# Kernel tuning notes

Hardware: AMD Instinct MI355X
Metric: run time of the kernel (lower is better)

## Reference

```python
import jax, jax.numpy as jnp
import numpy as np

# Model dims
B, S, D = 4, 2048, 2048   # batch, seq, emb_dim
E, K, M = 8, 2, 1024      # num_experts, num_experts_per_tok, intermediate_dim


def setup_inputs() -> dict:
    key = jax.random.key(0)
    k0, k1, k2, k3, k4 = jax.random.split(key, 5)
    d_scale = D ** -0.5
    m_scale = M ** -0.5
    return {
        "x": jax.random.normal(k0, (B, S, D), jnp.float32),
        "w_gate": jax.random.normal(k1, (D, E), jnp.float32) * d_scale,
        "wi_0": jax.random.normal(k2, (E, D, M), jnp.float32) * d_scale,  # gate proj per expert
        "wi_1": jax.random.normal(k3, (E, D, M), jnp.float32) * d_scale,  # up proj per expert
        "wo": jax.random.normal(k4, (E, M, D), jnp.float32) * m_scale,    # down proj per expert
    }


def reference(x, w_gate, wi_0, wi_1, wo):
    b, s, d = x.shape
    e = w_gate.shape[1]
    xf = x.reshape(-1, d)                       # [T, D], T = B*S
    # --- gate logits + top-k routing ---
    logits = jnp.dot(xf, w_gate)                # [T, E]
    top_logits, top_idx = jax.lax.top_k(logits, K)    # [T, K]
    weights = jax.nn.softmax(top_logits, axis=-1)     # [T, K] router weights
    # --- sort token copies by assigned expert (dispatch) ---
    flat_idx = top_idx.reshape(-1)              # [T*K] expert id per token copy
    sort_order = jnp.argsort(flat_idx)          # [T*K] dispatch permutation
    token_ids = sort_order // K                 # source token for each sorted slot
    sorted_x = jnp.take(xf, token_ids, axis=0)  # [T*K, D] gathered activations
    group_sizes = jnp.bincount(flat_idx, length=E).astype(jnp.int32)  # tokens per expert
    # --- grouped expert GEMMs (silu-gated MLP) ---
    h0 = jax.lax.ragged_dot(sorted_x, wi_0, group_sizes)  # [T*K, M]
    h1 = jax.lax.ragged_dot(sorted_x, wi_1, group_sizes)  # [T*K, M]
    inter = jax.nn.silu(h0) * h1
    out_sorted = jax.lax.ragged_dot(inter, wo, group_sizes)  # [T*K, D]
    # --- unsort + weighted combine ---
    unsort = jnp.argsort(sort_order)
    out = jnp.take(out_sorted, unsort, axis=0).reshape(-1, K, d)  # [T, K, D]
    out = jnp.einsum("tkd,tk->td", out, weights)
    return out.reshape(b, s, d)
```

## Files before the change

kernel.cpp:

```cpp
#include <hip/hip_runtime.h>
#include <hip/hip_bf16.h>
#include <math.h>

#define T_TOK 8192
#define DIM   2048
#define NE    8
#define MDIM  1024
#define TK    16384
#define CAP   (TK + 256)
#define MAXT  72

typedef __attribute__((ext_vector_type(8))) short bf16x8;
typedef __attribute__((ext_vector_type(4))) float f32x4;

typedef __attribute__((address_space(3))) unsigned char* lds_ptr_t;
typedef const __attribute__((address_space(1))) unsigned char* glb_ptr_t;

__device__ __forceinline__ unsigned short f2bf(float f) {
  union { float f; unsigned u; } v; v.f = f;
  unsigned r = v.u + 0x7fffu + ((v.u >> 16) & 1u);
  return (unsigned short)(r >> 16);
}

__device__ __forceinline__ void gload_lds16(const void* g, void* l) {
  __builtin_amdgcn_global_load_lds((glb_ptr_t)g, (lds_ptr_t)l, 16, 0, 0);
}

#define VM_FENCE(n) asm volatile("s_waitcnt vmcnt(" #n ")" ::: "memory")
#define BARRIER() __builtin_amdgcn_s_barrier()

__device__ __forceinline__ void stage_unit(const unsigned short* __restrict__ src,
                                           int ld, unsigned char* lds, int tid) {
#pragma unroll
  for (int j = 0; j < 2; j++) {
    int idx = j * 512 + tid;
    int row = idx >> 3;
    int gslot = (idx & 7) ^ (row & 7);
    gload_lds16(src + (size_t)row * ld + gslot * 8, lds + ((idx & ~63) << 4));
  }
}

__device__ __forceinline__ bf16x8 ldsfrag(const unsigned char* base, int row, int kb) {
  return *(const bf16x8*)(base + row * 128 + (kb ^ ((row & 7) << 4)));
}

__global__ __launch_bounds__(256) void router_kernel(
    const float* __restrict__ x, const float* __restrict__ wg,
    int* __restrict__ tok_eid, float* __restrict__ tok_w) {
  __shared__ float wgT[NE][1024];
  int tid = threadIdx.x;
  int wave = tid >> 6, lane = tid & 63;
  int t0 = blockIdx.x * 16 + wave * 4;

  double acc[4][NE];
#pragma unroll
  for (int tt = 0; tt < 4; tt++)
#pragma unroll
    for (int e = 0; e < NE; e++) acc[tt][e] = 0.0;

  for (int p = 0; p < 2; p++) {
    __syncthreads();
#pragma unroll
    for (int j = tid; j < 2048; j += 256) {
      float4 v = ((const float4*)wg)[p * 2048 + j];
      int d = j >> 1, h = (j & 1) * 4;
      wgT[h + 0][d] = v.x;
      wgT[h + 1][d] = v.y;
      wgT[h + 2][d] = v.z;
      wgT[h + 3][d] = v.w;
    }
    __syncthreads();
#pragma unroll
    for (int it = 0; it < 4; it++) {
      int dd = it * 256 + lane * 4;
      int gd = p * 1024 + dd;
      float4 wf[NE];
#pragma unroll
      for (int e = 0; e < NE; e++) wf[e] = *(const float4*)&wgT[e][dd];
#pragma unroll
      for (int tt = 0; tt < 4; tt++) {
        float4 xv = *(const float4*)(x + (size_t)(t0 + tt) * DIM + gd);
#pragma unroll
        for (int e = 0; e < NE; e++) {
          acc[tt][e] += (double)xv.x * (double)wf[e].x;
          acc[tt][e] += (double)xv.y * (double)wf[e].y;
          acc[tt][e] += (double)xv.z * (double)wf[e].z;
          acc[tt][e] += (double)xv.w * (double)wf[e].w;
        }
      }
    }
  }
#pragma unroll
  for (int tt = 0; tt < 4; tt++)
#pragma unroll
    for (int e = 0; e < NE; e++) {
      double v = acc[tt][e];
#pragma unroll
      for (int off = 32; off > 0; off >>= 1) v += __shfl_down(v, off, 64);
      acc[tt][e] = v;
    }
  if (lane == 0) {
#pragma unroll
    for (int tt = 0; tt < 4; tt++) {
      int t = t0 + tt;
      int b0 = 0; double l0 = acc[tt][0];
#pragma unroll
      for (int e = 1; e < NE; e++) { if (acc[tt][e] > l0) { l0 = acc[tt][e]; b0 = e; } }
      int b1 = -1; double l1 = -1.0e300;
#pragma unroll
      for (int e = 0; e < NE; e++) { if (e != b0 && acc[tt][e] > l1) { l1 = acc[tt][e]; b1 = e; } }
      double w0 = 1.0 / (1.0 + exp(l1 - l0));
      tok_eid[2 * t]     = b0;
      tok_eid[2 * t + 1] = b1;
      tok_w[2 * t]     = (float)w0;
      tok_w[2 * t + 1] = (float)(1.0 - w0);
    }
  }
}

__global__ __launch_bounds__(256) void plan_kernel(
    const int* __restrict__ tok_eid, int* __restrict__ offsets,
    int* __restrict__ tstart, int* __restrict__ tok_slot) {
  __shared__ int cnt[256][NE];
  __shared__ int pre[256][NE];
  __shared__ int tot[NE];
  __shared__ int off_sh[NE + 1];
  int th = threadIdx.x;
  int c[NE];
#pragma unroll
  for (int k = 0; k < NE; k++) c[k] = 0;
  for (int i = 0; i < TK / 256; i++) {
    int e = tok_eid[i * 256 + th];
#pragma unroll
    for (int k = 0; k < NE; k++) c[k] += (e == k) ? 1 : 0;
  }
#pragma unroll
  for (int k = 0; k < NE; k++) cnt[th][k] = c[k];
  __syncthreads();
  if (th < NE) {
    int run = 0;
#pragma unroll 4
    for (int i = 0; i < 256; i++) { pre[i][th] = run; run += cnt[i][th]; }
    tot[th] = run;
  }
  __syncthreads();
  if (th == 0) {
    int s = 0, ts = 0;
    for (int e = 0; e < NE; e++) {
      off_sh[e] = s; offsets[e] = s; s += tot[e];
      tstart[e] = ts; ts += (tot[e] + 255) / 256;
    }
    offsets[NE] = s; off_sh[NE] = s; tstart[NE] = ts;
  }
  __syncthreads();
  int b[NE];
#pragma unroll
  for (int k = 0; k < NE; k++) b[k] = off_sh[k] + pre[th][k];
  for (int i = 0; i < TK / 256; i++) {
    int idx = i * 256 + th;
    int e = tok_eid[idx];
    int slot = 0;
#pragma unroll
    for (int k = 0; k < NE; k++) {
      slot = (e == k) ? b[k] : slot;
      b[k] += (e == k) ? 1 : 0;
    }
    tok_slot[idx] = slot;
  }
}

__global__ __launch_bounds__(256) void dispatch_kernel(
    const float* __restrict__ x, const int* __restrict__ tok_slot,
    unsigned short* __restrict__ sorted_x) {
  int t = blockIdx.x;
  size_t s0 = (size_t)tok_slot[2 * t] * DIM;
  size_t s1 = (size_t)tok_slot[2 * t + 1] * DIM;
  const float4* xr = (const float4*)(x + (size_t)t * DIM);
#pragma unroll
  for (int i = threadIdx.x; i < DIM / 4; i += 256) {
    float4 v = xr[i];
    ushort4 b;
    b.x = f2bf(v.x); b.y = f2bf(v.y); b.z = f2bf(v.z); b.w = f2bf(v.w);
    *(ushort4*)(sorted_x + s0 + (size_t)i * 4) = b;
    *(ushort4*)(sorted_x + s1 + (size_t)i * 4) = b;
  }
}

__global__ __launch_bounds__(256) void transpose_cast_kernel(
    const float* __restrict__ in, unsigned short* __restrict__ out, int R, int C) {
  __shared__ unsigned short tile[32][33];
  int e = blockIdx.z;
  const float* inp = in + (size_t)e * R * C;
  unsigned short* outp = out + (size_t)e * R * C;
  int c0 = blockIdx.x * 32, r0 = blockIdx.y * 32;
  int tx = threadIdx.x & 31, ty = threadIdx.x >> 5;
#pragma unroll
  for (int i = 0; i < 32; i += 8)
    tile[ty + i][tx] = f2bf(inp[(size_t)(r0 + ty + i) * C + (c0 + tx)]);
  __syncthreads();
#pragma unroll
  for (int i = 0; i < 32; i += 8)
    outp[(size_t)(c0 + ty + i) * R + (r0 + tx)] = tile[tx][ty + i];
}

__global__ __launch_bounds__(512, 2) void gemm12_kernel(
    const unsigned short* __restrict__ A, const unsigned short* __restrict__ W0t,
    const unsigned short* __restrict__ W1t, const int* __restrict__ offsets,
    const int* __restrict__ tstart, unsigned short* __restrict__ inter) {
  extern __shared__ unsigned char smem[];
  int bx = blockIdx.x;
  if (bx >= tstart[NE]) return;
  int e = 0;
#pragma unroll
  for (int k = 1; k < NE; k++) if (tstart[k] <= bx) e = k;
  int row0 = offsets[e], row_end = offsets[e + 1];
  int tile_r0 = row0 + (bx - tstart[e]) * 256;
  if (tile_r0 >= row_end) return;
  int colb = blockIdx.y * 128;

  int tid = threadIdx.x;
  int wave = tid >> 6, lane = tid & 63;
  int wm = wave >> 2, wn = wave & 3;
  int l15 = lane & 15, grp16 = (lane >> 4) * 16;

  const unsigned short* Ab = A + (size_t)tile_r0 * DIM;
  const unsigned short* B0b = W0t + ((size_t)e * MDIM + colb) * DIM;
  const unsigned short* B1b = W1t + ((size_t)e * MDIM + colb) * DIM;

  f32x4 acc0[8][2], acc1[8][2];
#pragma unroll
  for (int i = 0; i < 8; i++)
#pragma unroll
    for (int j = 0; j < 2; j++) {
      acc0[i][j] = (f32x4){0.f, 0.f, 0.f, 0.f};
      acc1[i][j] = (f32x4){0.f, 0.f, 0.f, 0.f};
    }
  bf16x8 af[4][2], b0f[2][2], b1f[2][2];

  stage_unit(Ab, DIM, smem + 0, tid);
  stage_unit(B0b, DIM, smem + 32768, tid);
  stage_unit(B1b, DIM, smem + 49152, tid);
  stage_unit(Ab + (size_t)128 * DIM, DIM, smem + 16384, tid);
  VM_FENCE(4);
  BARRIER();

  for (int t = 0; t < 32; t++) {
    unsigned char* S = smem + (t & 1) * 65536;
    unsigned char* P = smem + ((t & 1) ^ 1) * 65536;
    int kn = (t < 31 ? t + 1 : t) * 64;
#pragma unroll
    for (int mi = 0; mi < 4; mi++) {
      int r = wm * 64 + mi * 16 + l15;
#pragma unroll
      for (int ks = 0; ks < 2; ks++) af[mi][ks] = ldsfrag(S, r, ks * 64 + grp16);
    }
#pragma unroll
    for (int ni = 0; ni < 2; ni++) {
      int r = wn * 32 + ni * 16 + l15;
#pragma unroll
      for (int ks = 0; ks < 2; ks++) b0f[ni][ks] = ldsfrag(S + 32768, r, ks * 64 + grp16);
    }
    stage_unit(Ab + kn, DIM, P, tid);
    BARRIER();
    __builtin_amdgcn_s_setprio(1);
#pragma unroll
    for (int ks = 0; ks < 2; ks++)
#pragma unroll
      for (int mi = 0; mi < 4; mi++)
#pragma unroll
        for (int ni = 0; ni < 2; ni++)
          acc0[mi][ni] = __builtin_amdgcn_mfma_f32_16x16x32_bf16(af[mi][ks], b0f[ni][ks], acc0[mi][ni], 0, 0, 0);
    __builtin_amdgcn_s_setprio(0);
    VM_FENCE(4);
    BARRIER();
#pragma unroll
    for (int ni = 0; ni < 2; ni++) {
      int r = wn * 32 + ni * 16 + l15;
#pragma unroll
      for (int ks = 0; ks < 2; ks++) b1f[ni][ks] = ldsfrag(S + 49152, r, ks * 64 + grp16);
    }
    stage_unit(B0b + kn, DIM, P + 32768, tid);
    BARRIER();
    __builtin_amdgcn_s_setprio(1);
#pragma unroll
    for (int ks = 0; ks < 2; ks++)
#pragma unroll
      for (int mi = 0; mi < 4; mi++)
#pragma unroll
        for (int ni = 0; ni < 2; ni++)
          acc1[mi][ni] = __builtin_amdgcn_mfma_f32_16x16x32_bf16(af[mi][ks], b1f[ni][ks], acc1[mi][ni], 0, 0, 0);
    __builtin_amdgcn_s_setprio(0);
    VM_FENCE(4);
    BARRIER();
#pragma unroll
    for (int mi = 0; mi < 4; mi++) {
      int r = 128 + wm * 64 + mi * 16 + l15;
#pragma unroll
      for (int ks = 0; ks < 2; ks++) af[mi][ks] = ldsfrag(S, r, ks * 64 + grp16);
    }
    stage_unit(B1b + kn, DIM, P + 49152, tid);
    BARRIER();
    __builtin_amdgcn_s_setprio(1);
#pragma unroll
    for (int ks = 0; ks < 2; ks++)
#pragma unroll
      for (int mi = 0; mi < 4; mi++)
#pragma unroll
        for (int ni = 0; ni < 2; ni++)
          acc0[4 + mi][ni] = __builtin_amdgcn_mfma_f32_16x16x32_bf16(af[mi][ks], b0f[ni][ks], acc0[4 + mi][ni], 0, 0, 0);
    __builtin_amdgcn_s_setprio(0);
    BARRIER();
    stage_unit(Ab + (size_t)128 * DIM + kn, DIM, P + 16384, tid);
    BARRIER();
    __builtin_amdgcn_s_setprio(1);
#pragma unroll
    for (int ks = 0; ks < 2; ks++)
#pragma unroll
      for (int mi = 0; mi < 4; mi++)
#pragma unroll
        for (int ni = 0; ni < 2; ni++)
          acc1[4 + mi][ni] = __builtin_amdgcn_mfma_f32_16x16x32_bf16(af[mi][ks], b1f[ni][ks], acc1[4 + mi][ni], 0, 0, 0);
    __builtin_amdgcn_s_setprio(0);
    VM_FENCE(4);
    BARRIER();
  }
  VM_FENCE(0);

#pragma unroll
  for (int half = 0; half < 2; half++)
#pragma unroll
    for (int mi = 0; mi < 4; mi++)
#pragma unroll
      for (int reg = 0; reg < 4; reg++) {
        int grow = tile_r0 + half * 128 + wm * 64 + mi * 16 + (lane >> 4) * 4 + reg;
        if (grow < row_end) {
#pragma unroll
          for (int ni = 0; ni < 2; ni++) {
            float h0 = acc0[half * 4 + mi][ni][reg];
            float h1 = acc1[half * 4 + mi][ni][reg];
            float g = h0 / (1.0f + __expf(-h0));
            inter[(size_t)grow * MDIM + colb + wn * 32 + ni * 16 + l15] = f2bf(g * h1);
          }
        }
      }
}

__global__ __launch_bounds__(512, 2) void gemm3_kernel(
    const unsigned short* __restrict__ A, const unsigned short* __restrict__ Wot,
    const int* __restrict__ offsets, const int* __restrict__ tstart,
    float* __restrict__ out_sorted) {
  extern __shared__ unsigned char smem[];
  int bx = blockIdx.x;
  if (bx >= tstart[NE]) return;
  int e = 0;
#pragma unroll
  for (int k = 1; k < NE; k++) if (tstart[k] <= bx) e = k;
  int row0 = offsets[e], row_end = offsets[e + 1];
  int tile_r0 = row0 + (bx - tstart[e]) * 256;
  if (tile_r0 >= row_end) return;
  int col0 = blockIdx.y * 256;

  int tid = threadIdx.x;
  int wave = tid >> 6, lane = tid & 63;
  int wm = wave >> 2, wn = wave & 3;
  int l15 = lane & 15, grp16 = (lane >> 4) * 16;

  const unsigned short* Ab = A + (size_t)tile_r0 * MDIM;
  const unsigned short* Bb = Wot + ((size_t)e * DIM + col0) * MDIM;

  f32x4 acc[8][4];
#pragma unroll
  for (int i = 0; i < 8; i++)
#pragma unroll
    for (int j = 0; j < 4; j++) acc[i][j] = (f32x4){0.f, 0.f, 0.f, 0.f};
  bf16x8 af[4][2], bfr[4][2];

  stage_unit(Ab, MDIM, smem + 0, tid);
  stage_unit(Bb, MDIM, smem + 32768, tid);
  stage_unit(Bb + (size_t)128 * MDIM, MDIM, smem + 49152, tid);
  stage_unit(Ab + (size_t)128 * MDIM, MDIM, smem + 16384, tid);
  VM_FENCE(4);
  BARRIER();

  for (int t = 0; t < 16; t++) {
    unsigned char* S = smem + (t & 1) * 65536;
    unsigned char* P = smem + ((t & 1) ^ 1) * 65536;
    int kn = (t < 15 ? t + 1 : t) * 64;
#pragma unroll
    for (int mi = 0; mi < 4; mi++) {
      int r = wm * 64 + mi * 16 + l15;
#pragma unroll
      for (int ks = 0; ks < 2; ks++) af[mi][ks] = ldsfrag(S, r, ks * 64 + grp16);
    }
#pragma unroll
    for (int ni = 0; ni < 2; ni++) {
      int r = wn * 32 + ni * 16 + l15;
#pragma unroll
      for (int ks = 0; ks < 2; ks++) bfr[ni][ks] = ldsfrag(S + 32768, r, ks * 64 + grp16);
    }
    stage_unit(Ab + kn, MDIM, P, tid);
    BARRIER();
    __builtin_amdgcn_s_setprio(1);
#pragma unroll
    for (int ks = 0; ks < 2; ks++)
#pragma unroll
      for (int mi = 0; mi < 4; mi++)
#pragma unroll
        for (int ni = 0; ni < 2; ni++)
          acc[mi][ni] = __builtin_amdgcn_mfma_f32_16x16x32_bf16(af[mi][ks], bfr[ni][ks], acc[mi][ni], 0, 0, 0);
    __builtin_amdgcn_s_setprio(0);
    VM_FENCE(4);
    BARRIER();
#pragma unroll
    for (int ni = 0; ni < 2; ni++) {
      int r = 128 + wn * 32 + ni * 16 + l15;
#pragma unroll
      for (int ks = 0; ks < 2; ks++) bfr[2 + ni][ks] = ldsfrag(S + 32768, r, ks * 64 + grp16);
    }
    stage_unit(Bb + kn, MDIM, P + 32768, tid);
    BARRIER();
    __builtin_amdgcn_s_setprio(1);
#pragma unroll
    for (int ks = 0; ks < 2; ks++)
#pragma unroll
      for (int mi = 0; mi < 4; mi++)
#pragma unroll
        for (int ni = 0; ni < 2; ni++)
          acc[mi][2 + ni] = __builtin_amdgcn_mfma_f32_16x16x32_bf16(af[mi][ks], bfr[2 + ni][ks], acc[mi][2 + ni], 0, 0, 0);
    __builtin_amdgcn_s_setprio(0);
    VM_FENCE(4);
    BARRIER();
#pragma unroll
    for (int mi = 0; mi < 4; mi++) {
      int r = 128 + wm * 64 + mi * 16 + l15;
#pragma unroll
      for (int ks = 0; ks < 2; ks++) af[mi][ks] = ldsfrag(S, r, ks * 64 + grp16);
    }
    stage_unit(Bb + (size_t)128 * MDIM + kn, MDIM, P + 49152, tid);
    BARRIER();
    __builtin_amdgcn_s_setprio(1);
#pragma unroll
    for (int ks = 0; ks < 2; ks++)
#pragma unroll
      for (int mi = 0; mi < 4; mi++)
#pragma unroll
        for (int ni = 0; ni < 2; ni++)
          acc[4 + mi][ni] = __builtin_amdgcn_mfma_f32_16x16x32_bf16(af[mi][ks], bfr[ni][ks], acc[4 + mi][ni], 0, 0, 0);
    __builtin_amdgcn_s_setprio(0);
    BARRIER();
    stage_unit(Ab + (size_t)128 * MDIM + kn, MDIM, P + 16384, tid);
    BARRIER();
    __builtin_amdgcn_s_setprio(1);
#pragma unroll
    for (int ks = 0; ks < 2; ks++)
#pragma unroll
      for (int mi = 0; mi < 4; mi++)
#pragma unroll
        for (int ni = 0; ni < 2; ni++)
          acc[4 + mi][2 + ni] = __builtin_amdgcn_mfma_f32_16x16x32_bf16(af[mi][ks], bfr[2 + ni][ks], acc[4 + mi][2 + ni], 0, 0, 0);
    __builtin_amdgcn_s_setprio(0);
    VM_FENCE(4);
    BARRIER();
  }
  VM_FENCE(0);

#pragma unroll
  for (int mh = 0; mh < 2; mh++)
#pragma unroll
    for (int mi = 0; mi < 4; mi++)
#pragma unroll
      for (int reg = 0; reg < 4; reg++) {
        int grow = tile_r0 + mh * 128 + wm * 64 + mi * 16 + (lane >> 4) * 4 + reg;
        if (grow < row_end) {
#pragma unroll
          for (int nh = 0; nh < 2; nh++) {
            float* orow = out_sorted + (size_t)grow * DIM + col0 + nh * 128 + wn * 32 + l15;
#pragma unroll
            for (int ni = 0; ni < 2; ni++)
              orow[ni * 16] = acc[mh * 4 + mi][nh * 2 + ni][reg];
          }
        }
      }
}

__global__ __launch_bounds__(256) void combine_kernel(
    const float* __restrict__ os, const int* __restrict__ tok_slot,
    const float* __restrict__ tok_w, float* __restrict__ out) {
  int t = blockIdx.x * 4 + (threadIdx.x >> 6);
  int lane = threadIdx.x & 63;
  int s0 = tok_slot[2 * t], s1 = tok_slot[2 * t + 1];
  float w0 = tok_w[2 * t], w1 = tok_w[2 * t + 1];
  const float4* a = (const float4*)(os + (size_t)s0 * DIM);
  const float4* b = (const float4*)(os + (size_t)s1 * DIM);
  float4* o = (float4*)(out + (size_t)t * DIM);
#pragma unroll
  for (int i = lane; i < DIM / 4; i += 64) {
    float4 va = a[i], vb = b[i];
    float4 r;
    r.x = w0 * va.x + w1 * vb.x;
    r.y = w0 * va.y + w1 * vb.y;
    r.z = w0 * va.z + w1 * vb.z;
    r.w = w0 * va.w + w1 * vb.w;
    o[i] = r;
  }
}

extern "C" void kernel_launch(void* const* d_in, const int* in_sizes, int n_in,
                              void* d_out, int out_size, void* d_ws, size_t ws_size,
                              hipStream_t stream) {
  const float* x   = (const float*)d_in[0];
  const float* wg  = (const float*)d_in[1];
  const float* wi0 = (const float*)d_in[2];
  const float* wi1 = (const float*)d_in[3];
  const float* wo  = (const float*)d_in[4];
  float* out = (float*)d_out;

  (void)hipFuncSetAttribute(reinterpret_cast<const void*>(gemm12_kernel),
                            hipFuncAttributeMaxDynamicSharedMemorySize, 131072);
  (void)hipFuncSetAttribute(reinterpret_cast<const void*>(gemm3_kernel),
                            hipFuncAttributeMaxDynamicSharedMemorySize, 131072);

  char* ws = (char*)d_ws;
  size_t off = 0;
  auto alloc = [&](size_t bytes) -> void* {
    void* p = ws + off;
    off = (off + bytes + 255) & ~(size_t)255;
    return p;
  };
  int*   offsets  = (int*)alloc((NE + 1) * 4);
  int*   tstart   = (int*)alloc((NE + 1) * 4);
  int*   tok_eid  = (int*)alloc((size_t)2 * T_TOK * 4);
  float* tok_w    = (float*)alloc((size_t)2 * T_TOK * 4);
  int*   tok_slot = (int*)alloc((size_t)2 * T_TOK * 4);
  unsigned short* inter    = (unsigned short*)alloc((size_t)CAP * MDIM * 2);
  unsigned short* sorted_x = (unsigned short*)alloc((size_t)CAP * DIM * 2);
  unsigned short* W0t      = (unsigned short*)alloc((size_t)NE * MDIM * DIM * 2);
  unsigned short* W1t      = (unsigned short*)alloc((size_t)NE * MDIM * DIM * 2);
  unsigned short* Wot      = (unsigned short*)alloc((size_t)NE * DIM * MDIM * 2);
  float* out_sorted = (float*)sorted_x;

  router_kernel<<<T_TOK / 16, 256, 0, stream>>>(x, wg, tok_eid, tok_w);
  plan_kernel<<<1, 256, 0, stream>>>(tok_eid, offsets, tstart, tok_slot);
  dispatch_kernel<<<T_TOK, 256, 0, stream>>>(x, tok_slot, sorted_x);
  transpose_cast_kernel<<<dim3(MDIM / 32, DIM / 32, NE), 256, 0, stream>>>(wi0, W0t, DIM, MDIM);
  transpose_cast_kernel<<<dim3(MDIM / 32, DIM / 32, NE), 256, 0, stream>>>(wi1, W1t, DIM, MDIM);
  transpose_cast_kernel<<<dim3(DIM / 32, MDIM / 32, NE), 256, 0, stream>>>(wo, Wot, MDIM, DIM);

  gemm12_kernel<<<dim3(MAXT, MDIM / 128, 1), 512, 131072, stream>>>(
      sorted_x, W0t, W1t, offsets, tstart, inter);
  gemm3_kernel<<<dim3(MAXT, DIM / 256, 1), 512, 131072, stream>>>(
      inter, Wot, offsets, tstart, out_sorted);
  combine_kernel<<<T_TOK / 4, 256, 0, stream>>>(out_sorted, tok_slot, tok_w, out);
}
```

Before: 614.7 us.

## Split tail row tiles into 64-row sub-tiles to balance the expert GEMM wave

Both expert GEMM kernels now launch on a flat 1D grid. The first 512 blocks cover row tiles 0-63 with the original 256-row pipelined path. Row tiles 64 and up, the per-expert padding overflow, are handled by blocks that each compute a 64-row quarter tile with a simpler single-stage double-buffered loop. The aim is to shrink the second wave of full-size tiles that ran after the first 512 blocks filled the device. In exchange the tail blocks reuse weights less and use a less overlapped load/compute schedule.

Result: faster. 590.3 us (-4.0%).

```diff
diff --git a/kernel.cpp b/kernel.cpp
--- a/kernel.cpp
+++ b/kernel.cpp
@@ -8,7 +8,6 @@
 #define MDIM  1024
 #define TK    16384
 #define CAP   (TK + 256)
-#define MAXT  72
 
 typedef __attribute__((ext_vector_type(8))) short bf16x8;
 typedef __attribute__((ext_vector_type(4))) float f32x4;
@@ -38,6 +37,13 @@
     int gslot = (idx & 7) ^ (row & 7);
     gload_lds16(src + (size_t)row * ld + gslot * 8, lds + ((idx & ~63) << 4));
   }
+}
+
+__device__ __forceinline__ void stage_unit64(const unsigned short* __restrict__ src,
+                                             int ld, unsigned char* lds, int tid) {
+  int row = tid >> 3;
+  int gslot = (tid & 7) ^ (row & 7);
+  gload_lds16(src + (size_t)row * ld + gslot * 8, lds + ((tid & ~63) << 4));
 }
 
 __device__ __forceinline__ bf16x8 ldsfrag(const unsigned char* base, int row, int kb) {
@@ -209,140 +215,226 @@
     const int* __restrict__ tstart, unsigned short* __restrict__ inter) {
   extern __shared__ unsigned char smem[];
   int bx = blockIdx.x;
-  if (bx >= tstart[NE]) return;
-  int e = 0;
-#pragma unroll
-  for (int k = 1; k < NE; k++) if (tstart[k] <= bx) e = k;
-  int row0 = offsets[e], row_end = offsets[e + 1];
-  int tile_r0 = row0 + (bx - tstart[e]) * 256;
-  if (tile_r0 >= row_end) return;
-  int colb = blockIdx.y * 128;
-
   int tid = threadIdx.x;
   int wave = tid >> 6, lane = tid & 63;
   int wm = wave >> 2, wn = wave & 3;
   int l15 = lane & 15, grp16 = (lane >> 4) * 16;
 
-  const unsigned short* Ab = A + (size_t)tile_r0 * DIM;
-  const unsigned short* B0b = W0t + ((size_t)e * MDIM + colb) * DIM;
-  const unsigned short* B1b = W1t + ((size_t)e * MDIM + colb) * DIM;
-
-  f32x4 acc0[8][2], acc1[8][2];
-#pragma unroll
-  for (int i = 0; i < 8; i++)
-#pragma unroll
-    for (int j = 0; j < 2; j++) {
-      acc0[i][j] = (f32x4){0.f, 0.f, 0.f, 0.f};
-      acc1[i][j] = (f32x4){0.f, 0.f, 0.f, 0.f};
-    }
-  bf16x8 af[4][2], b0f[2][2], b1f[2][2];
-
-  stage_unit(Ab, DIM, smem + 0, tid);
-  stage_unit(B0b, DIM, smem + 32768, tid);
-  stage_unit(B1b, DIM, smem + 49152, tid);
-  stage_unit(Ab + (size_t)128 * DIM, DIM, smem + 16384, tid);
-  VM_FENCE(4);
-  BARRIER();
-
-  for (int t = 0; t < 32; t++) {
-    unsigned char* S = smem + (t & 1) * 65536;
-    unsigned char* P = smem + ((t & 1) ^ 1) * 65536;
-    int kn = (t < 31 ? t + 1 : t) * 64;
-#pragma unroll
-    for (int mi = 0; mi < 4; mi++) {
-      int r = wm * 64 + mi * 16 + l15;
-#pragma unroll
-      for (int ks = 0; ks < 2; ks++) af[mi][ks] = ldsfrag(S, r, ks * 64 + grp16);
-    }
-#pragma unroll
-    for (int ni = 0; ni < 2; ni++) {
-      int r = wn * 32 + ni * 16 + l15;
-#pragma unroll
-      for (int ks = 0; ks < 2; ks++) b0f[ni][ks] = ldsfrag(S + 32768, r, ks * 64 + grp16);
-    }
-    stage_unit(Ab + kn, DIM, P, tid);
-    BARRIER();
-    __builtin_amdgcn_s_setprio(1);
-#pragma unroll
-    for (int ks = 0; ks < 2; ks++)
-#pragma unroll
-      for (int mi = 0; mi < 4; mi++)
-#pragma unroll
-        for (int ni = 0; ni < 2; ni++)
-          acc0[mi][ni] = __builtin_amdgcn_mfma_f32_16x16x32_bf16(af[mi][ks], b0f[ni][ks], acc0[mi][ni], 0, 0, 0);
-    __builtin_amdgcn_s_setprio(0);
+  if (bx < 512) {
+    int rt = bx >> 3;
+    int colb = (bx & 7) * 128;
+    int e = 0;
+#pragma unroll
+    for (int k = 1; k < NE; k++) if (tstart[k] <= rt) e = k;
+    int row_end = offsets[e + 1];
+    int tile_r0 = offsets[e] + (rt - tstart[e]) * 256;
+
+    const unsigned short* Ab = A + (size_t)tile_r0 * DIM;
+    const unsigned short* B0b = W0t + ((size_t)e * MDIM + colb) * DIM;
+    const unsigned short* B1b = W1t + ((size_t)e * MDIM + colb) * DIM;
+
+    f32x4 acc0[8][2], acc1[8][2];
+#pragma unroll
+    for (int i = 0; i < 8; i++)
+#pragma unroll
+      for (int j = 0; j < 2; j++) {
+        acc0[i][j] = (f32x4){0.f, 0.f, 0.f, 0.f};
+        acc1[i][j] = (f32x4){0.f, 0.f, 0.f, 0.f};
+      }
+    bf16x8 af[4][2], b0f[2][2], b1f[2][2];
+
+    stage_unit(Ab, DIM, smem + 0, tid);
+    stage_unit(B0b, DIM, smem + 32768, tid);
+    stage_unit(B1b, DIM, smem + 49152, tid);
+    stage_unit(Ab + (size_t)128 * DIM, DIM, smem + 16384, tid);
     VM_FENCE(4);
     BARRIER();
-#pragma unroll
-    for (int ni = 0; ni < 2; ni++) {
-      int r = wn * 32 + ni * 16 + l15;
-#pragma unroll
-      for (int ks = 0; ks < 2; ks++) b1f[ni][ks] = ldsfrag(S + 49152, r, ks * 64 + grp16);
-    }
-    stage_unit(B0b + kn, DIM, P + 32768, tid);
-    BARRIER();
-    __builtin_amdgcn_s_setprio(1);
-#pragma unroll
-    for (int ks = 0; ks < 2; ks++)
+
+    for (int t = 0; t < 32; t++) {
+      unsigned char* S = smem + (t & 1) * 65536;
+      unsigned char* P = smem + ((t & 1) ^ 1) * 65536;
+      int kn = (t < 31 ? t + 1 : t) * 64;
+#pragma unroll
+      for (int mi = 0; mi < 4; mi++) {
+        int r = wm * 64 + mi * 16 + l15;
+#pragma unroll
+        for (int ks = 0; ks < 2; ks++) af[mi][ks] = ldsfrag(S, r, ks * 64 + grp16);
+      }
+#pragma unroll
+      for (int ni = 0; ni < 2; ni++) {
+        int r = wn * 32 + ni * 16 + l15;
+#pragma unroll
+        for (int ks = 0; ks < 2; ks++) b0f[ni][ks] = ldsfrag(S + 32768, r, ks * 64 + grp16);
+      }
+      stage_unit(Ab + kn, DIM, P, tid);
+      BARRIER();
+      __builtin_amdgcn_s_setprio(1);
+#pragma unroll
+      for (int ks = 0; ks < 2; ks++)
+#pragma unroll
+        for (int mi = 0; mi < 4; mi++)
+#pragma unroll
+          for (int ni = 0; ni < 2; ni++)
+            acc0[mi][ni] = __builtin_amdgcn_mfma_f32_16x16x32_bf16(af[mi][ks], b0f[ni][ks], acc0[mi][ni], 0, 0, 0);
+      __builtin_amdgcn_s_setprio(0);
+      VM_FENCE(4);
+      BARRIER();
+#pragma unroll
+      for (int ni = 0; ni < 2; ni++) {
+        int r = wn * 32 + ni * 16 + l15;
+#pragma unroll
+        for (int ks = 0; ks < 2; ks++) b1f[ni][ks] = ldsfrag(S + 49152, r, ks * 64 + grp16);
+      }
+      stage_unit(B0b + kn, DIM, P + 32768, tid);
+      BARRIER();
+      __builtin_amdgcn_s_setprio(1);
+#pragma unroll
+      for (int ks = 0; ks < 2; ks++)
+#pragma unroll
+        for (int mi = 0; mi < 4; mi++)
+#pragma unroll
+          for (int ni = 0; ni < 2; ni++)
+            acc1[mi][ni] = __builtin_amdgcn_mfma_f32_16x16x32_bf16(af[mi][ks], b1f[ni][ks], acc1[mi][ni], 0, 0, 0);
+      __builtin_amdgcn_s_setprio(0);
+      VM_FENCE(4);
+      BARRIER();
+#pragma unroll
+      for (int mi = 0; mi < 4; mi++) {
+        int r = 128 + wm * 64 + mi * 16 + l15;
+#pragma unroll
+        for (int ks = 0; ks < 2; ks++) af[mi][ks] = ldsfrag(S, r, ks * 64 + grp16);
+      }
+      stage_unit(B1b + kn, DIM, P + 49152, tid);
+      BARRIER();
+      __builtin_amdgcn_s_setprio(1);
+#pragma unroll
+      for (int ks = 0; ks < 2; ks++)
+#pragma unroll
+        for (int mi = 0; mi < 4; mi++)
+#pragma unroll
+          for (int ni = 0; ni < 2; ni++)
+            acc0[4 + mi][ni] = __builtin_amdgcn_mfma_f32_16x16x32_bf16(af[mi][ks], b0f[ni][ks], acc0[4 + mi][ni], 0, 0, 0);
+      __builtin_amdgcn_s_setprio(0);
+      BARRIER();
+      stage_unit(Ab + (size_t)128 * DIM + kn, DIM, P + 16384, tid);
+      BARRIER();
+      __builtin_amdgcn_s_setprio(1);
+#pragma unroll
+      for (int ks = 0; ks < 2; ks++)
+#pragma unroll
+        for (int mi = 0; mi < 4; mi++)
+#pragma unroll
+          for (int ni = 0; ni < 2; ni++)
+            acc1[4 + mi][ni] = __builtin_amdgcn_mfma_f32_16x16x32_bf16(af[mi][ks], b1f[ni][ks], acc1[4 + mi][ni], 0, 0, 0);
+      __builtin_amdgcn_s_setprio(0);
+      VM_FENCE(4);
+      BARRIER();
+    }
+    VM_FENCE(0);
+
+#pragma unroll
+    for (int half = 0; half < 2; half++)
 #pragma unroll
       for (int mi = 0; mi < 4; mi++)
 #pragma unroll
-        for (int ni = 0; ni < 2; ni++)
-          acc1[mi][ni] = __builtin_amdgcn_mfma_f32_16x16x32_bf16(af[mi][ks], b1f[ni][ks], acc1[mi][ni], 0, 0, 0);
-    __builtin_amdgcn_s_setprio(0);
-    VM_FENCE(4);
-    BARRIER();
-#pragma unroll
-    for (int mi = 0; mi < 4; mi++) {
-      int r = 128 + wm * 64 + mi * 16 + l15;
-#pragma unroll
-      for (int ks = 0; ks < 2; ks++) af[mi][ks] = ldsfrag(S, r, ks * 64 + grp16);
-    }
-    stage_unit(B1b + kn, DIM, P + 49152, tid);
-    BARRIER();
-    __builtin_amdgcn_s_setprio(1);
-#pragma unroll
-    for (int ks = 0; ks < 2; ks++)
-#pragma unroll
-      for (int mi = 0; mi < 4; mi++)
-#pragma unroll
-        for (int ni = 0; ni < 2; ni++)
-          acc0[4 + mi][ni] = __builtin_amdgcn_mfma_f32_16x16x32_bf16(af[mi][ks], b0f[ni][ks], acc0[4 + mi][ni], 0, 0, 0);
-    __builtin_amdgcn_s_setprio(0);
-    BARRIER();
-    stage_unit(Ab + (size_t)128 * DIM + kn, DIM, P + 16384, tid);
-    BARRIER();
-    __builtin_amdgcn_s_setprio(1);
-#pragma unroll
-    for (int ks = 0; ks < 2; ks++)
-#pragma unroll
-      for (int mi = 0; mi < 4; mi++)
-#pragma unroll
-        for (int ni = 0; ni < 2; ni++)
-          acc1[4 + mi][ni] = __builtin_amdgcn_mfma_f32_16x16x32_bf16(af[mi][ks], b1f[ni][ks], acc1[4 + mi][ni], 0, 0, 0);
-    __builtin_amdgcn_s_setprio(0);
-    VM_FENCE(4);
-    BARRIER();
-  }
-  VM_FENCE(0);
-
-#pragma unroll
-  for (int half = 0; half < 2; half++)
-#pragma unroll
-    for (int mi = 0; mi < 4; mi++)
-#pragma unroll
-      for (int reg = 0; reg < 4; reg++) {
-        int grow = tile_r0 + half * 128 + wm * 64 + mi * 16 + (lane >> 4) * 4 + reg;
-        if (grow < row_end) {
-#pragma unroll
-          for (int ni = 0; ni < 2; ni++) {
-            float h0 = acc0[half * 4 + mi][ni][reg];
-            float h1 = acc1[half * 4 + mi][ni][reg];
-            float g = h0 / (1.0f + __expf(-h0));
-            inter[(size_t)grow * MDIM + colb + wn * 32 + ni * 16 + l15] = f2bf(g * h1);
+        for (int reg = 0; reg < 4; reg++) {
+          int grow = tile_r0 + half * 128 + wm * 64 + mi * 16 + (lane >> 4) * 4 + reg;
+          if (grow < row_end) {
+#pragma unroll
+            for (int ni = 0; ni < 2; ni++) {
+              float h0 = acc0[half * 4 + mi][ni][reg];
+              float h1 = acc1[half * 4 + mi][ni][reg];
+              float g = h0 / (1.0f + __expf(-h0));
+              inter[(size_t)grow * MDIM + colb + wn * 32 + ni * 16 + l15] = f2bf(g * h1);
+            }
           }
         }
-      }
+  } else {
+    int g = bx - 512;
+    int rt = 64 + (g >> 5);
+    if (rt >= tstart[NE]) return;
+    int q = (g >> 3) & 3;
+    int colb = (g & 7) * 128;
+    int e = 0;
+#pragma unroll
+    for (int k = 1; k < NE; k++) if (tstart[k] <= rt) e = k;
+    int row_end = offsets[e + 1];
+    int tr0 = offsets[e] + (rt - tstart[e]) * 256 + q * 64;
+    if (tr0 >= row_end) return;
+
+    const unsigned short* Ab = A + (size_t)tr0 * DIM;
+    const unsigned short* B0b = W0t + ((size_t)e * MDIM + colb) * DIM;
+    const unsigned short* B1b = W1t + ((size_t)e * MDIM + colb) * DIM;
+
+    f32x4 acc0[2][2], acc1[2][2];
+#pragma unroll
+    for (int i = 0; i < 2; i++)
+#pragma unroll
+      for (int j = 0; j < 2; j++) {
+        acc0[i][j] = (f32x4){0.f, 0.f, 0.f, 0.f};
+        acc1[i][j] = (f32x4){0.f, 0.f, 0.f, 0.f};
+      }
+    bf16x8 af[2][2], b0f[2][2], b1f[2][2];
+
+    stage_unit64(Ab, DIM, smem + 0, tid);
+    stage_unit(B0b, DIM, smem + 16384, tid);
+    stage_unit(B1b, DIM, smem + 49152, tid);
+    VM_FENCE(0);
+    BARRIER();
+
+    for (int t = 0; t < 32; t++) {
+      unsigned char* S = smem + (t & 1) * 65536;
+      unsigned char* P = smem + ((t & 1) ^ 1) * 65536;
+      int kn = (t < 31 ? t + 1 : t) * 64;
+      stage_unit64(Ab + kn, DIM, P, tid);
+      stage_unit(B0b + kn, DIM, P + 16384, tid);
+      stage_unit(B1b + kn, DIM, P + 49152, tid);
+#pragma unroll
+      for (int mi = 0; mi < 2; mi++) {
+        int r = wm * 32 + mi * 16 + l15;
+#pragma unroll
+        for (int ks = 0; ks < 2; ks++) af[mi][ks] = ldsfrag(S, r, ks * 64 + grp16);
+      }
+#pragma unroll
+      for (int ni = 0; ni < 2; ni++) {
+        int r = wn * 32 + ni * 16 + l15;
+#pragma unroll
+        for (int ks = 0; ks < 2; ks++) {
+          b0f[ni][ks] = ldsfrag(S + 16384, r, ks * 64 + grp16);
+          b1f[ni][ks] = ldsfrag(S + 49152, r, ks * 64 + grp16);
+        }
+      }
+      __builtin_amdgcn_s_setprio(1);
+#pragma unroll
+      for (int ks = 0; ks < 2; ks++)
+#pragma unroll
+        for (int mi = 0; mi < 2; mi++)
+#pragma unroll
+          for (int ni = 0; ni < 2; ni++) {
+            acc0[mi][ni] = __builtin_amdgcn_mfma_f32_16x16x32_bf16(af[mi][ks], b0f[ni][ks], acc0[mi][ni], 0, 0, 0);
+            acc1[mi][ni] = __builtin_amdgcn_mfma_f32_16x16x32_bf16(af[mi][ks], b1f[ni][ks], acc1[mi][ni], 0, 0, 0);
+          }
+      __builtin_amdgcn_s_setprio(0);
+      VM_FENCE(0);
+      BARRIER();
+    }
+
+#pragma unroll
+    for (int mi = 0; mi < 2; mi++)
+#pragma unroll
+      for (int reg = 0; reg < 4; reg++) {
+        int grow = tr0 + wm * 32 + mi * 16 + (lane >> 4) * 4 + reg;
+        if (grow < row_end) {
+#pragma unroll
+          for (int ni = 0; ni < 2; ni++) {
+            float h0 = acc0[mi][ni][reg];
+            float h1 = acc1[mi][ni][reg];
+            float gq = h0 / (1.0f + __expf(-h0));
+            inter[(size_t)grow * MDIM + colb + wn * 32 + ni * 16 + l15] = f2bf(gq * h1);
+          }
+        }
+      }
+  }
 }
 
 __global__ __launch_bounds__(512, 2) void gemm3_kernel(
@@ -351,136 +443,211 @@
     float* __restrict__ out_sorted) {
   extern __shared__ unsigned char smem[];
   int bx = blockIdx.x;
-  if (bx >= tstart[NE]) return;
-  int e = 0;
-#pragma unroll
-  for (int k = 1; k < NE; k++) if (tstart[k] <= bx) e = k;
-  int row0 = offsets[e], row_end = offsets[e + 1];
-  int tile_r0 = row0 + (bx - tstart[e]) * 256;
-  if (tile_r0 >= row_end) return;
-  int col0 = blockIdx.y * 256;
-
   int tid = threadIdx.x;
   int wave = tid >> 6, lane = tid & 63;
   int wm = wave >> 2, wn = wave & 3;
   int l15 = lane & 15, grp16 = (lane >> 4) * 16;
 
-  const unsigned short* Ab = A + (size_t)tile_r0 * MDIM;
-  const unsigned short* Bb = Wot + ((size_t)e * DIM + col0) * MDIM;
-
-  f32x4 acc[8][4];
-#pragma unroll
-  for (int i = 0; i < 8; i++)
-#pragma unroll
-    for (int j = 0; j < 4; j++) acc[i][j] = (f32x4){0.f, 0.f, 0.f, 0.f};
-  bf16x8 af[4][2], bfr[4][2];
-
-  stage_unit(Ab, MDIM, smem + 0, tid);
-  stage_unit(Bb, MDIM, smem + 32768, tid);
-  stage_unit(Bb + (size_t)128 * MDIM, MDIM, smem + 49152, tid);
-  stage_unit(Ab + (size_t)128 * MDIM, MDIM, smem + 16384, tid);
-  VM_FENCE(4);
-  BARRIER();
-
-  for (int t = 0; t < 16; t++) {
-    unsigned char* S = smem + (t & 1) * 65536;
-    unsigned char* P = smem + ((t & 1) ^ 1) * 65536;
-    int kn = (t < 15 ? t + 1 : t) * 64;
-#pragma unroll
-    for (int mi = 0; mi < 4; mi++) {
-      int r = wm * 64 + mi * 16 + l15;
-#pragma unroll
-      for (int ks = 0; ks < 2; ks++) af[mi][ks] = ldsfrag(S, r, ks * 64 + grp16);
-    }
-#pragma unroll
-    for (int ni = 0; ni < 2; ni++) {
-      int r = wn * 32 + ni * 16 + l15;
-#pragma unroll
-      for (int ks = 0; ks < 2; ks++) bfr[ni][ks] = ldsfrag(S + 32768, r, ks * 64 + grp16);
-    }
-    stage_unit(Ab + kn, MDIM, P, tid);
-    BARRIER();
-    __builtin_amdgcn_s_setprio(1);
-#pragma unroll
-    for (int ks = 0; ks < 2; ks++)
-#pragma unroll
-      for (int mi = 0; mi < 4; mi++)
-#pragma unroll
-        for (int ni = 0; ni < 2; ni++)
-          acc[mi][ni] = __builtin_amdgcn_mfma_f32_16x16x32_bf16(af[mi][ks], bfr[ni][ks], acc[mi][ni], 0, 0, 0);
-    __builtin_amdgcn_s_setprio(0);
+  if (bx < 512) {
+    int rt = bx >> 3;
+    int col0 = (bx & 7) * 256;
+    int e = 0;
+#pragma unroll
+    for (int k = 1; k < NE; k++) if (tstart[k] <= rt) e = k;
+    int row_end = offsets[e + 1];
+    int tile_r0 = offsets[e] + (rt - tstart[e]) * 256;
+
+    const unsigned short* Ab = A + (size_t)tile_r0 * MDIM;
+    const unsigned short* Bb = Wot + ((size_t)e * DIM + col0) * MDIM;
+
+    f32x4 acc[8][4];
+#pragma unroll
+    for (int i = 0; i < 8; i++)
+#pragma unroll
+      for (int j = 0; j < 4; j++) acc[i][j] = (f32x4){0.f, 0.f, 0.f, 0.f};
+    bf16x8 af[4][2], bfr[4][2];
+
+    stage_unit(Ab, MDIM, smem + 0, tid);
+    stage_unit(Bb, MDIM, smem + 32768, tid);
+    stage_unit(Bb + (size_t)128 * MDIM, MDIM, smem + 49152, tid);
+    stage_unit(Ab + (size_t)128 * MDIM, MDIM, smem + 16384, tid);
     VM_FENCE(4);
     BARRIER();
-#pragma unroll
-    for (int ni = 0; ni < 2; ni++) {
-      int r = 128 + wn * 32 + ni * 16 + l15;
-#pragma unroll
-      for (int ks = 0; ks < 2; ks++) bfr[2 + ni][ks] = ldsfrag(S + 32768, r, ks * 64 + grp16);
-    }
-    stage_unit(Bb + kn, MDIM, P + 32768, tid);
-    BARRIER();
-    __builtin_amdgcn_s_setprio(1);
-#pragma unroll
-    for (int ks = 0; ks < 2; ks++)
+
+    for (int t = 0; t < 16; t++) {
+      unsigned char* S = smem + (t & 1) * 65536;
+      unsigned char* P = smem + ((t & 1) ^ 1) * 65536;
+      int kn = (t < 15 ? t + 1 : t) * 64;
+#pragma unroll
+      for (int mi = 0; mi < 4; mi++) {
+        int r = wm * 64 + mi * 16 + l15;
+#pragma unroll
+        for (int ks = 0; ks < 2; ks++) af[mi][ks] = ldsfrag(S, r, ks * 64 + grp16);
+      }
+#pragma unroll
+      for (int ni = 0; ni < 2; ni++) {
+        int r = wn * 32 + ni * 16 + l15;
+#pragma unroll
+        for (int ks = 0; ks < 2; ks++) bfr[ni][ks] = ldsfrag(S + 32768, r, ks * 64 + grp16);
+      }
+      stage_unit(Ab + kn, MDIM, P, tid);
+      BARRIER();
+      __builtin_amdgcn_s_setprio(1);
+#pragma unroll
+      for (int ks = 0; ks < 2; ks++)
+#pragma unroll
+        for (int mi = 0; mi < 4; mi++)
+#pragma unroll
+          for (int ni = 0; ni < 2; ni++)
+            acc[mi][ni] = __builtin_amdgcn_mfma_f32_16x16x32_bf16(af[mi][ks], bfr[ni][ks], acc[mi][ni], 0, 0, 0);
+      __builtin_amdgcn_s_setprio(0);
+      VM_FENCE(4);
+      BARRIER();
+#pragma unroll
+      for (int ni = 0; ni < 2; ni++) {
+        int r = 128 + wn * 32 + ni * 16 + l15;
+#pragma unroll
+        for (int ks = 0; ks < 2; ks++) bfr[2 + ni][ks] = ldsfrag(S + 32768, r, ks * 64 + grp16);
+      }
+      stage_unit(Bb + kn, MDIM, P + 32768, tid);
+      BARRIER();
+      __builtin_amdgcn_s_setprio(1);
+#pragma unroll
+      for (int ks = 0; ks < 2; ks++)
+#pragma unroll
+        for (int mi = 0; mi < 4; mi++)
+#pragma unroll
+          for (int ni = 0; ni < 2; ni++)
+            acc[mi][2 + ni] = __builtin_amdgcn_mfma_f32_16x16x32_bf16(af[mi][ks], bfr[2 + ni][ks], acc[mi][2 + ni], 0, 0, 0);
+      __builtin_amdgcn_s_setprio(0);
+      VM_FENCE(4);
+      BARRIER();
+#pragma unroll
+      for (int mi = 0; mi < 4; mi++) {
+        int r = 128 + wm * 64 + mi * 16 + l15;
+#pragma unroll
+        for (int ks = 0; ks < 2; ks++) af[mi][ks] = ldsfrag(S, r, ks * 64 + grp16);
+      }
+      stage_unit(Bb + (size_t)128 * MDIM + kn, MDIM, P + 49152, tid);
+      BARRIER();
+      __builtin_amdgcn_s_setprio(1);
+#pragma unroll
+      for (int ks = 0; ks < 2; ks++)
+#pragma unroll
+        for (int mi = 0; mi < 4; mi++)
+#pragma unroll
+          for (int ni = 0; ni < 2; ni++)
+            acc[4 + mi][ni] = __builtin_amdgcn_mfma_f32_16x16x32_bf16(af[mi][ks], bfr[ni][ks], acc[4 + mi][ni], 0, 0, 0);
+      __builtin_amdgcn_s_setprio(0);
+      BARRIER();
+      stage_unit(Ab + (size_t)128 * MDIM + kn, MDIM, P + 16384, tid);
+      BARRIER();
+      __builtin_amdgcn_s_setprio(1);
+#pragma unroll
+      for (int ks = 0; ks < 2; ks++)
+#pragma unroll
+        for (int mi = 0; mi < 4; mi++)
+#pragma unroll
+          for (int ni = 0; ni < 2; ni++)
+            acc[4 + mi][2 + ni] = __builtin_amdgcn_mfma_f32_16x16x32_bf16(af[mi][ks], bfr[2 + ni][ks], acc[4 + mi][2 + ni], 0, 0, 0);
+      __builtin_amdgcn_s_setprio(0);
+      VM_FENCE(4);
+      BARRIER();
+    }
+    VM_FENCE(0);
+
+#pragma unroll
+    for (int mh = 0; mh < 2; mh++)
 #pragma unroll
       for (int mi = 0; mi < 4; mi++)
 #pragma unroll
-        for (int ni = 0; ni < 2; ni++)
-          acc[mi][2 + ni] = __builtin_amdgcn_mfma_f32_16x16x32_bf16(af[mi][ks], bfr[2 + ni][ks], acc[mi][2 + ni], 0, 0, 0);
-    __builtin_amdgcn_s_setprio(0);
-    VM_FENCE(4);
-    BARRIER();
-#pragma unroll
-    for (int mi = 0; mi < 4; mi++) {
-      int r = 128 + wm * 64 + mi * 16 + l15;
-#pragma unroll
-      for (int ks = 0; ks < 2; ks++) af[mi][ks] = ldsfrag(S, r, ks * 64 + grp16);
-    }
-    stage_unit(Bb + (size_t)128 * MDIM + kn, MDIM, P + 49152, tid);
-    BARRIER();
-    __builtin_amdgcn_s_setprio(1);
-#pragma unroll
-    for (int ks = 0; ks < 2; ks++)
-#pragma unroll
-      for (int mi = 0; mi < 4; mi++)
-#pragma unroll
-        for (int ni = 0; ni < 2; ni++)
-          acc[4 + mi][ni] = __builtin_amdgcn_mfma_f32_16x16x32_bf16(af[mi][ks], bfr[ni][ks], acc[4 + mi][ni], 0, 0, 0);
-    __builtin_amdgcn_s_setprio(0);
-    BARRIER();
-    stage_unit(Ab + (size_t)128 * MDIM + kn, MDIM, P + 16384, tid);
-    BARRIER();
-    __builtin_amdgcn_s_setprio(1);
-#pragma unroll
-    for (int ks = 0; ks < 2; ks++)
-#pragma unroll
-      for (int mi = 0; mi < 4; mi++)
-#pragma unroll
-        for (int ni = 0; ni < 2; ni++)
-          acc[4 + mi][2 + ni] = __builtin_amdgcn_mfma_f32_16x16x32_bf16(af[mi][ks], bfr[2 + ni][ks], acc[4 + mi][2 + ni], 0, 0, 0);
-    __builtin_amdgcn_s_setprio(0);
-    VM_FENCE(4);
-    BARRIER();
-  }
-  VM_FENCE(0);
-
-#pragma unroll
-  for (int mh = 0; mh < 2; mh++)
-#pragma unroll
-    for (int mi = 0; mi < 4; mi++)
-#pragma unroll
-      for (int reg = 0; reg < 4; reg++) {
-        int grow = tile_r0 + mh * 128 + wm * 64 + mi * 16 + (lane >> 4) * 4 + reg;
-        if (grow < row_end) {
-#pragma unroll
-          for (int nh = 0; nh < 2; nh++) {
-            float* orow = out_sorted + (size_t)grow * DIM + col0 + nh * 128 + wn * 32 + l15;
-#pragma unroll
-            for (int ni = 0; ni < 2; ni++)
-              orow[ni * 16] = acc[mh * 4 + mi][nh * 2 + ni][reg];
+        for (int reg = 0; reg < 4; reg++) {
+          int grow = tile_r0 + mh * 128 + wm * 64 + mi * 16 + (lane >> 4) * 4 + reg;
+          if (grow < row_end) {
+#pragma unroll
+            for (int nh = 0; nh < 2; nh++) {
+              float* orow = out_sorted + (size_t)grow * DIM + col0 + nh * 128 + wn * 32 + l15;
+#pragma unroll
+              for (int ni = 0; ni < 2; ni++)
+                orow[ni * 16] = acc[mh * 4 + mi][nh * 2 + ni][reg];
+            }
           }
         }
-      }
+  } else {
+    int g = bx - 512;
+    int rt = 64 + (g >> 5);
+    if (rt >= tstart[NE]) return;
+    int q = (g >> 3) & 3;
+    int col0 = (g & 7) * 256;
+    int e = 0;
+#pragma unroll
+    for (int k = 1; k < NE; k++) if (tstart[k] <= rt) e = k;
+    int row_end = offsets[e + 1];
+    int tr0 = offsets[e] + (rt - tstart[e]) * 256 + q * 64;
+    if (tr0 >= row_end) return;
+
+    const unsigned short* Ab = A + (size_t)tr0 * MDIM;
+    const unsigned short* Bb = Wot + ((size_t)e * DIM + col0) * MDIM;
+
+    f32x4 acc[2][4];
+#pragma unroll
+    for (int i = 0; i < 2; i++)
+#pragma unroll
+      for (int j = 0; j < 4; j++) acc[i][j] = (f32x4){0.f, 0.f, 0.f, 0.f};
+    bf16x8 af[2][2], bfr[4][2];
+
+    stage_unit64(Ab, MDIM, smem + 0, tid);
+    stage_unit(Bb, MDIM, smem + 16384, tid);
+    stage_unit(Bb + (size_t)128 * MDIM, MDIM, smem + 49152, tid);
+    VM_FENCE(0);
+    BARRIER();
+
+    for (int t = 0; t < 16; t++) {
+      unsigned char* S = smem + (t & 1) * 65536;
+      unsigned char* P = smem + ((t & 1) ^ 1) * 65536;
+      int kn = (t < 15 ? t + 1 : t) * 64;
+      stage_unit64(Ab + kn, MDIM, P, tid);
+      stage_unit(Bb + kn, MDIM, P + 16384, tid);
+      stage_unit(Bb + (size_t)128 * MDIM + kn, MDIM, P + 49152, tid);
+#pragma unroll
+      for (int mi = 0; mi < 2; mi++) {
+        int r = wm * 32 + mi * 16 + l15;
+#pragma unroll
+        for (int ks = 0; ks < 2; ks++) af[mi][ks] = ldsfrag(S, r, ks * 64 + grp16);
+      }
+#pragma unroll
+      for (int ni = 0; ni < 4; ni++) {
+        int r = wn * 64 + ni * 16 + l15;
+        const unsigned char* Bbase = (r < 128) ? (S + 16384) : (S + 32768);
+#pragma unroll
+        for (int ks = 0; ks < 2; ks++) bfr[ni][ks] = ldsfrag(Bbase, r, ks * 64 + grp16);
+      }
+      __builtin_amdgcn_s_setprio(1);
+#pragma unroll
+      for (int ks = 0; ks < 2; ks++)
+#pragma unroll
+        for (int mi = 0; mi < 2; mi++)
+#pragma unroll
+          for (int ni = 0; ni < 4; ni++)
+            acc[mi][ni] = __builtin_amdgcn_mfma_f32_16x16x32_bf16(af[mi][ks], bfr[ni][ks], acc[mi][ni], 0, 0, 0);
+      __builtin_amdgcn_s_setprio(0);
+      VM_FENCE(0);
+      BARRIER();
+    }
+
+#pragma unroll
+    for (int mi = 0; mi < 2; mi++)
+#pragma unroll
+      for (int reg = 0; reg < 4; reg++) {
+        int grow = tr0 + wm * 32 + mi * 16 + (lane >> 4) * 4 + reg;
+        if (grow < row_end) {
+          float* orow = out_sorted + (size_t)grow * DIM + col0 + wn * 64 + l15;
+#pragma unroll
+          for (int ni = 0; ni < 4; ni++)
+            orow[ni * 16] = acc[mi][ni][reg];
+        }
+      }
+  }
 }
 
 __global__ __launch_bounds__(256) void combine_kernel(
@@ -546,9 +713,9 @@
   transpose_cast_kernel<<<dim3(MDIM / 32, DIM / 32, NE), 256, 0, stream>>>(wi1, W1t, DIM, MDIM);
   transpose_cast_kernel<<<dim3(DIM / 32, MDIM / 32, NE), 256, 0, stream>>>(wo, Wot, MDIM, DIM);
 
-  gemm12_kernel<<<dim3(MAXT, MDIM / 128, 1), 512, 131072, stream>>>(
+  gemm12_kernel<<<dim3(768, 1, 1), 512, 131072, stream>>>(
       sorted_x, W0t, W1t, offsets, tstart, inter);
-  gemm3_kernel<<<dim3(MAXT, DIM / 256, 1), 512, 131072, stream>>>(
+  gemm3_kernel<<<dim3(768, 1, 1), 512, 131072, stream>>>(
       inter, Wot, offsets, tstart, out_sorted);
   combine_kernel<<<T_TOK / 4, 256, 0, stream>>>(out_sorted, tok_slot, tok_w, out);
 }
```
